# Optimization experiments

Hardware: AMD Instinct MI355X
Metric: run time of the kernel (lower is better)

## Reference

```python
import jax, jax.numpy as jnp
import numpy as np

N = 32        # number of parallel heads (MEME/Agent57 mixture size)
A = 18        # action_size (full Atari action set)
D = 512       # dim (module default)
B = 4096      # batch size


def setup_inputs() -> dict:
    key = jax.random.key(0)
    ks = jax.random.split(key, 10)
    s = 1.0 / np.sqrt(D)  # torch default init bound for fan_in = D (Linear and Conv1d with 1 in-ch * kernel D)
    u = lambda k, shape: jax.random.uniform(k, shape, jnp.float32, -s, s)
    x = jax.random.normal(ks[0], (B, D), jnp.float32)
    # linear1: dim -> N*dim
    W1 = u(ks[1], (N * D, D))
    b1 = u(ks[2], (N * D,))
    # linear2: grouped conv == N independent DxD linear maps
    W2 = u(ks[3], (N, D, D))   # [head, out_feat, in_feat]
    b2 = u(ks[4], (N, D))
    # value: N independent dot-products (D -> 1 per head)
    Wv = u(ks[5], (N, D))
    bv = u(ks[6], (N,))
    # adv: N independent D -> action_size maps
    Wa = u(ks[7], (N, A, D))
    ba = u(ks[8], (N, A))
    return {"x": x, "W1": W1, "b1": b1, "W2": W2, "b2": b2,
            "Wv": Wv, "bv": bv, "Wa": Wa, "ba": ba}


def reference(x, W1, b1, W2, b2, Wv, bv, Wa, ba):
    Bsz = x.shape[0]
    # linear1 then split into N heads: [B, N*D] -> [B, N, D]
    h = (x @ W1.T + b1).reshape(Bsz, N, D)
    # grouped conv (kernel_size=D, groups=N) == per-head DxD GEMM
    h2 = jnp.einsum('bnd,ned->bne', h, W2) + b2          # [B, N, D]
    # value head: per-head dot product -> [B, N, 1]
    v = jnp.einsum('bnd,nd->bn', h2, Wv) + bv            # [B, N]
    # advantage head: per-head D -> A map
    a = jnp.einsum('bnd,nad->bna', h2, Wa) + ba          # [B, N, A]
    # dueling combine: value + (adv - mean_adv)
    return v[..., None] + (a - jnp.mean(a, axis=-1, keepdims=True))
```

## Files before the change

kernel.cpp:

```cpp
#include <hip/hip_runtime.h>
#include <hip/hip_bf16.h>

#define DD   512
#define NH   32
#define AA   18
#define JJ   (NH*AA)
#define BB   4096
#define JD   (JJ*DD)

typedef short bf16x8 __attribute__((ext_vector_type(8)));
typedef float f32x4  __attribute__((ext_vector_type(4)));

static __device__ inline unsigned short f2bf(float f) {
    unsigned int x = __float_as_uint(f);
    unsigned int r = (x + 0x7fffu + ((x >> 16) & 1u)) >> 16;
    return (unsigned short)r;
}
static __device__ inline float bf2f(unsigned int bits) {
    return __uint_as_float(bits << 16);
}

__global__ __launch_bounds__(256) void k_V(
    const float* __restrict__ x, unsigned short* __restrict__ Xb,
    const float* __restrict__ W2, const float* __restrict__ Wv,
    const float* __restrict__ Wa, const float* __restrict__ b2,
    unsigned short* __restrict__ Vb, float* __restrict__ c1)
{
    const int t  = threadIdx.x;
    const int dc = blockIdx.x;
    const int n  = blockIdx.y;

    __shared__ __align__(16) unsigned short usb[32 * DD];
    __shared__ float redc[AA * 4];

    {
        const int bid = n*16 + dc;
        const float4* xin = (const float4*)x + (size_t)bid*1024;
        ushort4*      xo  = (ushort4*)Xb + (size_t)bid*1024;
        #pragma unroll
        for (int i = 0; i < 4; ++i) {
            const float4 v = xin[t + 256*i];
            ushort4 o;
            o.x = f2bf(v.x); o.y = f2bf(v.y); o.z = f2bf(v.z); o.w = f2bf(v.w);
            xo[t + 256*i] = o;
        }
    }

    {
        const int e = 2*t;
        float u0[AA], u1[AA];
        float msum0 = 0.f, msum1 = 0.f;
        #pragma unroll
        for (int a = 0; a < AA; ++a) {
            const float2 w = *(const float2*)(Wa + (size_t)(n*AA + a)*DD + e);
            u0[a] = w.x; u1[a] = w.y; msum0 += w.x; msum1 += w.y;
        }
        msum0 *= (1.0f/18.0f); msum1 *= (1.0f/18.0f);
        const float2 wv  = *(const float2*)(Wv + (size_t)n*DD + e);
        const float2 b2v = *(const float2*)(b2 + (size_t)n*DD + e);
        float p[AA];
        #pragma unroll
        for (int a = 0; a < AA; ++a) {
            u0[a] = wv.x + u0[a] - msum0;
            u1[a] = wv.y + u1[a] - msum1;
            const unsigned int pk = ((unsigned int)f2bf(u1[a]) << 16) | f2bf(u0[a]);
            const int slot = (t >> 2) ^ (a & 7);
            *(unsigned int*)(usb + a*DD + slot*8 + (t & 3)*2) = pk;
            p[a] = u0[a]*b2v.x + u1[a]*b2v.y;
        }
        if (dc == 0) {
            #pragma unroll
            for (int a = 0; a < AA; ++a)
                for (int o = 32; o; o >>= 1) p[a] += __shfl_xor(p[a], o, 64);
            if ((t & 63) == 0) {
                const int w = t >> 6;
                #pragma unroll
                for (int a = 0; a < AA; ++a) redc[a*4 + w] = p[a];
            }
            __syncthreads();
            if (t < AA)
                c1[n*AA + t] = redc[t*4] + redc[t*4+1] + redc[t*4+2] + redc[t*4+3];
        }
    }
    __syncthreads();

    const int lane = t & 63, w = t >> 6;
    const int wp = w & 1;
    const int wd = w >> 1;
    const int ln = lane & 15, lg = lane >> 4;
    const int d0 = dc*32 + wd*16;
    const int arow = wp*16 + ln;
    const float* w2base = W2 + (size_t)n*DD*DD + d0 + ln;

    f32x4 acc = {};
    #pragma unroll 2
    for (int kt = 0; kt < 16; ++kt) {
        const float* gp = w2base + (size_t)(kt*32 + lg*8)*DD;
        float wvv[8];
        #pragma unroll
        for (int j = 0; j < 8; ++j) wvv[j] = gp[(size_t)j*DD];
        bf16x8 bfrag;
        #pragma unroll
        for (int j = 0; j < 8; ++j) bfrag[j] = (short)f2bf(wvv[j]);
        const int slot = (kt*4 + lg) ^ (arow & 7);
        const bf16x8 afrag = *(const bf16x8*)(usb + arow*DD + slot*8);
        acc = __builtin_amdgcn_mfma_f32_16x16x32_bf16(afrag, bfrag, acc, 0, 0, 0);
    }

    #pragma unroll
    for (int r = 0; r < 4; ++r) {
        const int a = wp*16 + lg*4 + r;
        if (a < AA)
            Vb[(size_t)(n*AA + a)*DD + d0 + ln] = f2bf(acc[r]);
    }
}

__global__ __launch_bounds__(256) void k_M(
    const float* __restrict__ W1, const unsigned short* __restrict__ Vb,
    const float* __restrict__ b1, const float* __restrict__ bv,
    const float* __restrict__ ba, const float* __restrict__ c1,
    unsigned short* __restrict__ Mb, float* __restrict__ c3)
{
    const int t  = threadIdx.x;
    const int kc = blockIdx.x;
    const int n  = blockIdx.y;

    __shared__ __align__(16) unsigned short vsb[32 * DD];
    __shared__ float redc[AA * 4];

    for (int idx = t; idx < AA*64; idx += 256) {
        const int row = idx >> 6, slot = idx & 63;
        const int4 v = *(const int4*)(Vb + (size_t)(n*AA + row)*DD + slot*8);
        *(int4*)(vsb + row*DD + ((slot ^ (row & 7))*8)) = v;
    }
    __syncthreads();

    if (kc == 0) {
        const int e = 2*t;
        const float2 b1v = *(const float2*)(b1 + (size_t)n*DD + e);
        float p[AA];
        #pragma unroll
        for (int a = 0; a < AA; ++a) {
            const unsigned int pk = *(const unsigned int*)(Vb + (size_t)(n*AA + a)*DD + e);
            p[a] = bf2f(pk & 0xffffu)*b1v.x + bf2f(pk >> 16)*b1v.y;
        }
        #pragma unroll
        for (int a = 0; a < AA; ++a)
            for (int o = 32; o; o >>= 1) p[a] += __shfl_xor(p[a], o, 64);
        if ((t & 63) == 0) {
            const int w = t >> 6;
            #pragma unroll
            for (int a = 0; a < AA; ++a) redc[a*4 + w] = p[a];
        }
        __syncthreads();
        if (t < AA) {
            float bam = 0.f;
            #pragma unroll
            for (int a = 0; a < AA; ++a) bam += ba[n*AA + a];
            c3[n*AA + t] = c1[n*AA + t]
                         + redc[t*4] + redc[t*4+1] + redc[t*4+2] + redc[t*4+3]
                         + bv[n] + ba[n*AA + t] - bam * (1.0f/18.0f);
        }
    }

    const int lane = t & 63, w = t >> 6;
    const int wp = w & 1;
    const int wd = w >> 1;
    const int ln = lane & 15, lg = lane >> 4;
    const int k0 = kc*32 + wd*16;
    const int arow = wp*16 + ln;
    const float* w1base = W1 + (size_t)n*DD*DD + k0 + ln;

    f32x4 acc = {};
    #pragma unroll 2
    for (int kt = 0; kt < 16; ++kt) {
        const float* gp = w1base + (size_t)(kt*32 + lg*8)*DD;
        float wvv[8];
        #pragma unroll
        for (int j = 0; j < 8; ++j) wvv[j] = gp[(size_t)j*DD];
        bf16x8 bfrag;
        #pragma unroll
        for (int j = 0; j < 8; ++j) bfrag[j] = (short)f2bf(wvv[j]);
        const int slot = (kt*4 + lg) ^ (arow & 7);
        const bf16x8 afrag = *(const bf16x8*)(vsb + arow*DD + slot*8);
        acc = __builtin_amdgcn_mfma_f32_16x16x32_bf16(afrag, bfrag, acc, 0, 0, 0);
    }

    #pragma unroll
    for (int r = 0; r < 4; ++r) {
        const int a = wp*16 + lg*4 + r;
        if (a < AA)
            Mb[(size_t)(n*AA + a)*DD + k0 + ln] = f2bf(acc[r]);
    }
}

#define GBM 128
#define GBN 64
#define GBK 64

__global__ __launch_bounds__(256) void k_gemm(
    const unsigned short* __restrict__ Xb,
    const unsigned short* __restrict__ Mb,
    const float* __restrict__ c3, float* __restrict__ out)
{
    __shared__ __align__(16) unsigned short xs[GBM * GBK];
    __shared__ __align__(16) unsigned short ms[GBN * GBK];

    const int t    = threadIdx.x;
    const int w    = t >> 6;
    const int lane = t & 63;
    const int ln   = lane & 15, lg = lane >> 4;
    const int wm   = w >> 1,   wn = w & 1;
    const int b0 = blockIdx.x * GBM;
    const int j0 = blockIdx.y * GBN;

    f32x4 acc[4][2] = {};

    for (int kc = 0; kc < DD; kc += GBK) {
        #pragma unroll
        for (int it = 0; it < 4; ++it) {
            const int chunk = it*256 + t;
            const int row = chunk >> 3, slot = chunk & 7;
            const int4 v = *(const int4*)(Xb + (size_t)(b0 + row)*DD + kc + slot*8);
            *(int4*)(xs + row*GBK + ((slot ^ (row & 7)) * 8)) = v;
        }
        #pragma unroll
        for (int it = 0; it < 2; ++it) {
            const int chunk = it*256 + t;
            const int row = chunk >> 3, slot = chunk & 7;
            const int4 v = *(const int4*)(Mb + (size_t)(j0 + row)*DD + kc + slot*8);
            *(int4*)(ms + row*GBK + ((slot ^ (row & 7)) * 8)) = v;
        }
        __syncthreads();

        #pragma unroll
        for (int kk = 0; kk < 2; ++kk) {
            bf16x8 av[4], bv[2];
            #pragma unroll
            for (int mt = 0; mt < 4; ++mt) {
                const int row  = 64*wm + 16*mt + ln;
                const int slot = (4*kk + lg) ^ (row & 7);
                av[mt] = *(const bf16x8*)(xs + row*GBK + slot*8);
            }
            #pragma unroll
            for (int nt = 0; nt < 2; ++nt) {
                const int row  = 32*wn + 16*nt + ln;
                const int slot = (4*kk + lg) ^ (row & 7);
                bv[nt] = *(const bf16x8*)(ms + row*GBK + slot*8);
            }
            #pragma unroll
            for (int mt = 0; mt < 4; ++mt)
                #pragma unroll
                for (int nt = 0; nt < 2; ++nt)
                    acc[mt][nt] = __builtin_amdgcn_mfma_f32_16x16x32_bf16(
                        av[mt], bv[nt], acc[mt][nt], 0, 0, 0);
        }
        __syncthreads();
    }

    float c3v[2];
    #pragma unroll
    for (int nt = 0; nt < 2; ++nt) c3v[nt] = c3[j0 + 32*wn + 16*nt + ln];

    #pragma unroll
    for (int mt = 0; mt < 4; ++mt)
        #pragma unroll
        for (int nt = 0; nt < 2; ++nt) {
            const int j = j0 + 32*wn + 16*nt + ln;
            #pragma unroll
            for (int r = 0; r < 4; ++r) {
                const int b = b0 + 64*wm + 16*mt + 4*lg + r;
                out[(size_t)b*JJ + j] = acc[mt][nt][r] + c3v[nt];
            }
        }
}

extern "C" void kernel_launch(void* const* d_in, const int* in_sizes, int n_in,
                              void* d_out, int out_size, void* d_ws, size_t ws_size,
                              hipStream_t stream)
{
    const float* x  = (const float*)d_in[0];
    const float* W1 = (const float*)d_in[1];
    const float* b1 = (const float*)d_in[2];
    const float* W2 = (const float*)d_in[3];
    const float* b2 = (const float*)d_in[4];
    const float* Wv = (const float*)d_in[5];
    const float* bv = (const float*)d_in[6];
    const float* Wa = (const float*)d_in[7];
    const float* ba = (const float*)d_in[8];
    float* out = (float*)d_out;
    float* ws  = (float*)d_ws;

    float* c1 = ws;
    float* c3 = c1 + JJ;
    unsigned short* Xb = (unsigned short*)(c3 + JJ);
    unsigned short* Vb = Xb + (size_t)BB*DD;
    unsigned short* Mb = Vb + (size_t)JD;

    k_V   <<<dim3(16, NH), 256, 0, stream>>>(x, Xb, W2, Wv, Wa, b2, Vb, c1);
    k_M   <<<dim3(16, NH), 256, 0, stream>>>(W1, Vb, b1, bv, ba, c1, Mb, c3);
    k_gemm<<<dim3(BB/GBM, JJ/GBN), 256, 0, stream>>>(Xb, Mb, c3, out);
}
```

Baseline: 37.41 us.

## Fuse x bf16 conversion into final GEMM and shrink its M tile

Moves the fp32-to-bf16 conversion of x out of the first kernel and into the final GEMM's shared-memory load, so the bf16 copy of x is never written to or read back from the workspace. The final GEMM tile drops from 128 to 64 rows, doubling the block count and halving the accumulator registers. The W2/W1 loops in the first two kernels are unrolled by 4 instead of 2. In exchange, each x element is now read as fp32 and converted once per N-tile block (9 times), and each block does less MFMA work per Mb load.

```diff
diff --git a/kernel.cpp b/kernel.cpp
--- a/kernel.cpp
+++ b/kernel.cpp
@@ -16,12 +16,11 @@
     unsigned int r = (x + 0x7fffu + ((x >> 16) & 1u)) >> 16;
     return (unsigned short)r;
 }
-static __device__ inline float bf2f(unsigned int bits) {
-    return __uint_as_float(bits << 16);
+static __device__ inline float bf2f(unsigned short bits) {
+    return __uint_as_float((unsigned int)bits << 16);
 }
 
 __global__ __launch_bounds__(256) void k_V(
-    const float* __restrict__ x, unsigned short* __restrict__ Xb,
     const float* __restrict__ W2, const float* __restrict__ Wv,
     const float* __restrict__ Wa, const float* __restrict__ b2,
     unsigned short* __restrict__ Vb, float* __restrict__ c1)
@@ -32,19 +31,6 @@
 
     __shared__ __align__(16) unsigned short usb[32 * DD];
     __shared__ float redc[AA * 4];
-
-    {
-        const int bid = n*16 + dc;
-        const float4* xin = (const float4*)x + (size_t)bid*1024;
-        ushort4*      xo  = (ushort4*)Xb + (size_t)bid*1024;
-        #pragma unroll
-        for (int i = 0; i < 4; ++i) {
-            const float4 v = xin[t + 256*i];
-            ushort4 o;
-            o.x = f2bf(v.x); o.y = f2bf(v.y); o.z = f2bf(v.z); o.w = f2bf(v.w);
-            xo[t + 256*i] = o;
-        }
-    }
 
     {
         const int e = 2*t;
@@ -93,7 +79,7 @@
     const float* w2base = W2 + (size_t)n*DD*DD + d0 + ln;
 
     f32x4 acc = {};
-    #pragma unroll 2
+    #pragma unroll 4
     for (int kt = 0; kt < 16; ++kt) {
         const float* gp = w2base + (size_t)(kt*32 + lg*8)*DD;
         float wvv[8];
@@ -142,7 +128,8 @@
         #pragma unroll
         for (int a = 0; a < AA; ++a) {
             const unsigned int pk = *(const unsigned int*)(Vb + (size_t)(n*AA + a)*DD + e);
-            p[a] = bf2f(pk & 0xffffu)*b1v.x + bf2f(pk >> 16)*b1v.y;
+            p[a] = bf2f((unsigned short)(pk & 0xffffu))*b1v.x
+                 + bf2f((unsigned short)(pk >> 16))*b1v.y;
         }
         #pragma unroll
         for (int a = 0; a < AA; ++a)
@@ -172,7 +159,7 @@
     const float* w1base = W1 + (size_t)n*DD*DD + k0 + ln;
 
     f32x4 acc = {};
-    #pragma unroll 2
+    #pragma unroll 4
     for (int kt = 0; kt < 16; ++kt) {
         const float* gp = w1base + (size_t)(kt*32 + lg*8)*DD;
         float wvv[8];
@@ -194,12 +181,12 @@
     }
 }
 
-#define GBM 128
+#define GBM 64
 #define GBN 64
 #define GBK 64
 
 __global__ __launch_bounds__(256) void k_gemm(
-    const unsigned short* __restrict__ Xb,
+    const float* __restrict__ x,
     const unsigned short* __restrict__ Mb,
     const float* __restrict__ c3, float* __restrict__ out)
 {
@@ -214,31 +201,33 @@
     const int b0 = blockIdx.x * GBM;
     const int j0 = blockIdx.y * GBN;
 
-    f32x4 acc[4][2] = {};
+    f32x4 acc[2][2] = {};
 
     for (int kc = 0; kc < DD; kc += GBK) {
-        #pragma unroll
-        for (int it = 0; it < 4; ++it) {
-            const int chunk = it*256 + t;
-            const int row = chunk >> 3, slot = chunk & 7;
-            const int4 v = *(const int4*)(Xb + (size_t)(b0 + row)*DD + kc + slot*8);
-            *(int4*)(xs + row*GBK + ((slot ^ (row & 7)) * 8)) = v;
-        }
         #pragma unroll
         for (int it = 0; it < 2; ++it) {
             const int chunk = it*256 + t;
             const int row = chunk >> 3, slot = chunk & 7;
-            const int4 v = *(const int4*)(Mb + (size_t)(j0 + row)*DD + kc + slot*8);
-            *(int4*)(ms + row*GBK + ((slot ^ (row & 7)) * 8)) = v;
+            const float* xp = x + (size_t)(b0 + row)*DD + kc + slot*8;
+            const float4 a0 = *(const float4*)(xp);
+            const float4 a1 = *(const float4*)(xp + 4);
+            int4 vv;
+            vv.x = (int)(((unsigned int)f2bf(a0.y) << 16) | f2bf(a0.x));
+            vv.y = (int)(((unsigned int)f2bf(a0.w) << 16) | f2bf(a0.z));
+            vv.z = (int)(((unsigned int)f2bf(a1.y) << 16) | f2bf(a1.x));
+            vv.w = (int)(((unsigned int)f2bf(a1.w) << 16) | f2bf(a1.z));
+            *(int4*)(xs + row*GBK + ((slot ^ (row & 7)) * 8)) = vv;
+            const int4 vm = *(const int4*)(Mb + (size_t)(j0 + row)*DD + kc + slot*8);
+            *(int4*)(ms + row*GBK + ((slot ^ (row & 7)) * 8)) = vm;
         }
         __syncthreads();
 
         #pragma unroll
         for (int kk = 0; kk < 2; ++kk) {
-            bf16x8 av[4], bv[2];
-            #pragma unroll
-            for (int mt = 0; mt < 4; ++mt) {
-                const int row  = 64*wm + 16*mt + ln;
+            bf16x8 av[2], bv[2];
+            #pragma unroll
+            for (int mt = 0; mt < 2; ++mt) {
+                const int row  = 32*wm + 16*mt + ln;
                 const int slot = (4*kk + lg) ^ (row & 7);
                 av[mt] = *(const bf16x8*)(xs + row*GBK + slot*8);
             }
@@ -249,7 +238,7 @@
                 bv[nt] = *(const bf16x8*)(ms + row*GBK + slot*8);
             }
             #pragma unroll
-            for (int mt = 0; mt < 4; ++mt)
+            for (int mt = 0; mt < 2; ++mt)
                 #pragma unroll
                 for (int nt = 0; nt < 2; ++nt)
                     acc[mt][nt] = __builtin_amdgcn_mfma_f32_16x16x32_bf16(
@@ -263,13 +252,13 @@
     for (int nt = 0; nt < 2; ++nt) c3v[nt] = c3[j0 + 32*wn + 16*nt + ln];
 
     #pragma unroll
-    for (int mt = 0; mt < 4; ++mt)
+    for (int mt = 0; mt < 2; ++mt)
         #pragma unroll
         for (int nt = 0; nt < 2; ++nt) {
             const int j = j0 + 32*wn + 16*nt + ln;
             #pragma unroll
             for (int r = 0; r < 4; ++r) {
-                const int b = b0 + 64*wm + 16*mt + 4*lg + r;
+                const int b = b0 + 32*wm + 16*mt + 4*lg + r;
                 out[(size_t)b*JJ + j] = acc[mt][nt][r] + c3v[nt];
             }
         }
@@ -293,11 +282,10 @@
 
     float* c1 = ws;
     float* c3 = c1 + JJ;
-    unsigned short* Xb = (unsigned short*)(c3 + JJ);
-    unsigned short* Vb = Xb + (size_t)BB*DD;
+    unsigned short* Vb = (unsigned short*)(c3 + JJ);
     unsigned short* Mb = Vb + (size_t)JD;
 
-    k_V   <<<dim3(16, NH), 256, 0, stream>>>(x, Xb, W2, Wv, Wa, b2, Vb, c1);
+    k_V   <<<dim3(16, NH), 256, 0, stream>>>(W2, Wv, Wa, b2, Vb, c1);
     k_M   <<<dim3(16, NH), 256, 0, stream>>>(W1, Vb, b1, bv, ba, c1, Mb, c3);
-    k_gemm<<<dim3(BB/GBM, JJ/GBN), 256, 0, stream>>>(Xb, Mb, c3, out);
-}
+    k_gemm<<<dim3(BB/GBM, JJ/GBN), 256, 0, stream>>>(x, Mb, c3, out);
+}
```

After: 39.52 us. +5.7%, slower.
